# Performance work log

Hardware: AMD Instinct MI355X
Metric: run time of the kernel (lower is better)

Reference implementation:

```python
import jax, jax.numpy as jnp
import numpy as np

EMBED_DIM = 1024
N_HEADS = 16
HEAD_DIM = EMBED_DIM // N_HEADS


def setup_inputs() -> dict:
    key = jax.random.key(0)
    k_x, k_wi, k_bi, k_wo, k_bo = jax.random.split(key, 5)
    B, N, C = 4, 2048, EMBED_DIM
    scale = 1.0 / np.sqrt(C)
    return {
        "x": jax.random.normal(k_x, (B, N, C), dtype=jnp.float32),
        "w_in": jax.random.normal(k_wi, (C, 3 * C), dtype=jnp.float32) * scale,
        "b_in": jax.random.normal(k_bi, (3 * C,), dtype=jnp.float32) * 0.01,
        "w_out": jax.random.normal(k_wo, (C, C), dtype=jnp.float32) * scale,
        "b_out": jax.random.normal(k_bo, (C,), dtype=jnp.float32) * 0.01,
    }


def reference(x, w_in, b_in, w_out, b_out):
    B, N, C = x.shape
    H, D = N_HEADS, HEAD_DIM
    qkv = x @ w_in + b_in  # (B, N, 3C)
    q, k, v = jnp.split(qkv, 3, axis=-1)
    # (B, H, N, D)
    q = q.reshape(B, N, H, D).transpose(0, 2, 1, 3)
    k = k.reshape(B, N, H, D).transpose(0, 2, 1, 3)
    v = v.reshape(B, N, H, D).transpose(0, 2, 1, 3)
    # Naive attention: full (B,H,N,N) scores, NO sqrt(d) scaling (as in source)
    scores = jnp.einsum("bhnd,bhmd->bhnm", q, k)
    attn = jax.nn.softmax(scores, axis=-1)
    out = jnp.einsum("bhnm,bhmd->bhnd", attn, v)
    out = out.transpose(0, 2, 1, 3).reshape(B, N, C)
    return out @ w_out + b_out
```

## Files before the change

### kernel.cpp

```cpp
#include <hip/hip_runtime.h>
#include <hip/hip_bf16.h>
#include <stdint.h>

typedef __attribute__((ext_vector_type(8))) __bf16 bf8v;
typedef __attribute__((ext_vector_type(4))) float f4v;

#define L2E 1.44269504088896f

__device__ __forceinline__ unsigned short f2bf(float f) {
  union { float f; unsigned u; } v; v.f = f;
  unsigned r = v.u + 0x7fffu + ((v.u >> 16) & 1u);
  return (unsigned short)(r >> 16);
}

__device__ __forceinline__ unsigned pk2bf(float f0, float f1) {
  union { __hip_bfloat162 h; unsigned u; } c;
  c.h = __float22bfloat162_rn(make_float2(f0, f1));
  return c.u;
}

__device__ __forceinline__ float exp2_hw(float x) {
  return __builtin_amdgcn_exp2f(x);
}

__device__ __forceinline__ void gl_lds16(const void* g, void* l) {
  __builtin_amdgcn_global_load_lds(
      (__attribute__((address_space(1))) void*)(g),
      (__attribute__((address_space(3))) void*)(l), 16, 0, 0);
}

__global__ void prep_kernel(const float* __restrict__ x,
                            const float* __restrict__ w_in,
                            const float* __restrict__ w_out,
                            unsigned short* __restrict__ xb,
                            unsigned short* __restrict__ wiT,
                            unsigned short* __restrict__ woT) {
  __shared__ float tile[32][33];
  int bx = blockIdx.x;
  if (bx < 8192) {
    int i = bx * 256 + threadIdx.x;
    float4 v = ((const float4*)x)[i];
    ushort4 o;
    o.x = f2bf(v.x); o.y = f2bf(v.y); o.z = f2bf(v.z); o.w = f2bf(v.w);
    ((ushort4*)xb)[i] = o;
    return;
  }
  int idx = bx - 8192;
  int bxx = idx & 127, byy = idx >> 7;
  const float* in; unsigned short* out; int C, c0;
  if (bxx < 96) { in = w_in;  out = wiT; C = 3072; c0 = bxx * 32; }
  else          { in = w_out; out = woT; C = 1024; c0 = (bxx - 96) * 32; }
  int r0 = byy * 32;
  int tx = threadIdx.x & 31, ty = threadIdx.x >> 5;
#pragma unroll
  for (int j = 0; j < 4; ++j)
    tile[ty + 8 * j][tx] = in[(size_t)(r0 + ty + 8 * j) * C + c0 + tx];
  __syncthreads();
#pragma unroll
  for (int j = 0; j < 4; ++j)
    out[(size_t)(c0 + ty + 8 * j) * 1024 + r0 + tx] = f2bf(tile[tx][ty + 8 * j]);
}

__global__ void transpose_v_kernel(const unsigned short* __restrict__ qkv,
                                   unsigned short* __restrict__ vtg) {
  __shared__ unsigned short tile[32][33];
  int bh = blockIdx.z;
  int d0 = blockIdx.y * 32;
  int n0 = blockIdx.x * 32;
  int b = bh >> 4, h = bh & 15;
  int tx = threadIdx.x, ty = threadIdx.y;
  const unsigned short* src = qkv + (size_t)b * 2048 * 3072 + 2048 + h * 64 + d0;
#pragma unroll
  for (int j = 0; j < 4; ++j)
    tile[ty + 8 * j][tx] = src[(size_t)(n0 + ty + 8 * j) * 3072 + tx];
  __syncthreads();
  unsigned short* dst = vtg + ((size_t)bh * 64) * 2048;
#pragma unroll
  for (int j = 0; j < 4; ++j)
    dst[(size_t)(d0 + ty + 8 * j) * 2048 + n0 + tx] = tile[tx][ty + 8 * j];
}

__global__ __launch_bounds__(512, 2) void gemm_bt256(
    const unsigned short* __restrict__ A,
    const unsigned short* __restrict__ BT,
    const float* __restrict__ bias,
    unsigned short* __restrict__ C,
    int N, int K, int nbx, int scale_ncols, float scale) {
  __shared__ __align__(16) unsigned short As[2][256 * 64];
  __shared__ __align__(16) unsigned short Bs[2][256 * 64];
  const int tid = threadIdx.x;
  const int wave = tid >> 6, lane = tid & 63;
  const int lo = lane & 15, hi = lane >> 4;
  const int wm = wave >> 2, wn = wave & 3;

  const int nwg = gridDim.x;
  const int cpx = nwg >> 3;
  const int s = (blockIdx.x & 7) * cpx + (blockIdx.x >> 3);
  const int by = s / nbx, bx = s - by * nbx;
  const int m0 = by * 256, n0 = bx * 256;

  const int srow = lane >> 3;
  const int scol = ((lane & 7) * 8) ^ ((lane >> 1) & 16);
  const unsigned short* gA = A + (size_t)(m0 + wave * 8 + srow) * K + scol;
  const unsigned short* gB = BT + (size_t)(n0 + wave * 8 + srow) * K + scol;

  const int colsw0 = (hi * 8) ^ ((lo & 4) << 2);
  const int colsw1 = (32 + hi * 8) ^ ((lo & 4) << 2);
  const int rA = wm * 128 + lo;
  const int rB = wn * 64 + lo;

  f4v acc[8][4] = {};
  const int nt = K >> 6;

#pragma unroll
  for (int j = 0; j < 4; ++j) {
    gl_lds16(gA + (size_t)(j * 64) * K, &As[0][(j * 64 + wave * 8) * 64]);
    gl_lds16(gB + (size_t)(j * 64) * K, &Bs[0][(j * 64 + wave * 8) * 64]);
  }

  for (int t = 0; t < nt; ++t) {
    const int c = t & 1;
    __builtin_amdgcn_s_barrier();
    __builtin_amdgcn_sched_barrier(0);
    if (t + 1 < nt) {
      const unsigned short* gA1 = gA + (size_t)(t + 1) * 64;
      const unsigned short* gB1 = gB + (size_t)(t + 1) * 64;
#pragma unroll
      for (int j = 0; j < 4; ++j) {
        gl_lds16(gA1 + (size_t)(j * 64) * K, &As[c ^ 1][(j * 64 + wave * 8) * 64]);
        gl_lds16(gB1 + (size_t)(j * 64) * K, &Bs[c ^ 1][(j * 64 + wave * 8) * 64]);
      }
      asm volatile("s_waitcnt vmcnt(8)" ::: "memory");
    } else {
      asm volatile("s_waitcnt vmcnt(0)" ::: "memory");
    }
    __builtin_amdgcn_sched_barrier(0);
    __builtin_amdgcn_s_barrier();
    __builtin_amdgcn_sched_barrier(0);

    bf8v b[4][2];
#pragma unroll
    for (int fn = 0; fn < 4; ++fn) {
      b[fn][0] = *(const bf8v*)&Bs[c][(rB + fn * 16) * 64 + colsw0];
      b[fn][1] = *(const bf8v*)&Bs[c][(rB + fn * 16) * 64 + colsw1];
    }
#pragma unroll
    for (int p = 0; p < 4; ++p) {
      bf8v a[2][2];
#pragma unroll
      for (int i = 0; i < 2; ++i) {
        a[i][0] = *(const bf8v*)&As[c][(rA + (p * 2 + i) * 16) * 64 + colsw0];
        a[i][1] = *(const bf8v*)&As[c][(rA + (p * 2 + i) * 16) * 64 + colsw1];
      }
      __builtin_amdgcn_s_setprio(1);
#pragma unroll
      for (int ks = 0; ks < 2; ++ks)
#pragma unroll
        for (int i = 0; i < 2; ++i)
#pragma unroll
          for (int fn = 0; fn < 4; ++fn)
            acc[p * 2 + i][fn] = __builtin_amdgcn_mfma_f32_16x16x32_bf16(
                a[i][ks], b[fn][ks], acc[p * 2 + i][fn], 0, 0, 0);
      __builtin_amdgcn_s_setprio(0);
    }
  }

#pragma unroll
  for (int i = 0; i < 8; ++i) {
#pragma unroll
    for (int r = 0; r < 4; ++r) {
      int row = m0 + wm * 128 + i * 16 + hi * 4 + r;
#pragma unroll
      for (int j = 0; j < 4; ++j) {
        int col = n0 + wn * 64 + j * 16 + lo;
        float v = acc[i][j][r] + bias[col];
        if (col < scale_ncols) v *= scale;
        C[(size_t)row * N + col] = f2bf(v);
      }
    }
  }
}

__global__ __launch_bounds__(256, 4) void gemm_bt_sm(
    const unsigned short* __restrict__ A,
    const unsigned short* __restrict__ BT,
    const float* __restrict__ bias,
    float* __restrict__ C,
    int M, int N, int K) {
  __shared__ __align__(16) unsigned short As[64 * 32];
  __shared__ __align__(16) unsigned short Bs[128 * 32];
  const int tid = threadIdx.x;
  const int wave = tid >> 6, lane = tid & 63;
  const int lo = lane & 15, hi = lane >> 4;
  const int m0 = blockIdx.y * 64, n0 = blockIdx.x * 128;
  const int wm = (wave >> 1) * 32, wn = (wave & 1) * 64;

  f4v acc[2][4] = {};

  const int srow = lane >> 2;
  const int scol = (lane & 3) * 8;

  for (int k0 = 0; k0 < K; k0 += 32) {
    gl_lds16(A + (size_t)(m0 + wave * 16 + srow) * K + k0 + scol,
             &As[(wave * 16) * 32]);
#pragma unroll
    for (int p = 0; p < 2; ++p) {
      int r = p * 64 + wave * 16 + srow;
      gl_lds16(BT + (size_t)(n0 + r) * K + k0 + scol,
               &Bs[(p * 64 + wave * 16) * 32]);
    }
    __syncthreads();
    bf8v a[2], b[4];
#pragma unroll
    for (int i = 0; i < 2; ++i)
      a[i] = *(const bf8v*)&As[(wm + i * 16 + lo) * 32 + hi * 8];
#pragma unroll
    for (int j = 0; j < 4; ++j)
      b[j] = *(const bf8v*)&Bs[(wn + j * 16 + lo) * 32 + hi * 8];
#pragma unroll
    for (int i = 0; i < 2; ++i)
#pragma unroll
      for (int j = 0; j < 4; ++j)
        acc[i][j] = __builtin_amdgcn_mfma_f32_16x16x32_bf16(a[i], b[j], acc[i][j], 0, 0, 0);
    __syncthreads();
  }

#pragma unroll
  for (int i = 0; i < 2; ++i) {
#pragma unroll
    for (int r = 0; r < 4; ++r) {
      int row = m0 + wm + i * 16 + hi * 4 + r;
#pragma unroll
      for (int j = 0; j < 4; ++j) {
        int col = n0 + wn + j * 16 + lo;
        C[(size_t)row * N + col] = acc[i][j][r] + bias[col];
      }
    }
  }
}

#define FSTR 72

__global__ __launch_bounds__(256, 2) void flash_attn(
    const unsigned short* __restrict__ qkv,
    const unsigned short* __restrict__ vtg,
    unsigned short* __restrict__ y) {
  __shared__ __align__(16) unsigned short Ps[256 * FSTR];
  __shared__ __align__(16) unsigned short Kt[64 * FSTR];
  __shared__ __align__(16) unsigned short Vt[64 * FSTR];
  const int tid = threadIdx.x;
  const int wave = tid >> 6, lane = tid & 63;
  const int lo = lane & 15, hi = lane >> 4;

  const int lin = blockIdx.x;
  const int swz = (lin & 7) * 64 + (lin >> 3);
  const int q0 = (swz & 7) << 8;
  const int h  = (swz >> 3) & 15;
  const int b  = swz >> 7;

  const size_t base = (size_t)b * 2048 * 3072;
  const int qoff = h * 64, koff = 1024 + h * 64;
  const unsigned short* vsrc = vtg + (size_t)(b * 16 + h) * 64 * 2048;

  const int m_st = tid >> 3, c_st = tid & 7;
  const unsigned short* kg = qkv + base + koff;
  float4 rk0, rk1, rv0, rv1;
  auto kv_load = [&](int kt) {
    const int mb = kt * 64;
    rk0 = *(const float4*)(kg + (size_t)(mb + m_st) * 3072 + c_st * 8);
    rk1 = *(const float4*)(kg + (size_t)(mb + m_st + 32) * 3072 + c_st * 8);
    rv0 = *(const float4*)(vsrc + (size_t)m_st * 2048 + mb + c_st * 8);
    rv1 = *(const float4*)(vsrc + (size_t)(m_st + 32) * 2048 + mb + c_st * 8);
  };
  auto kv_write = [&]() {
    *(float4*)&Kt[m_st * FSTR + c_st * 8] = rk0;
    *(float4*)&Kt[(m_st + 32) * FSTR + c_st * 8] = rk1;
    *(float4*)&Vt[m_st * FSTR + c_st * 8] = rv0;
    *(float4*)&Vt[(m_st + 32) * FSTR + c_st * 8] = rv1;
  };

  kv_load(0);

#pragma unroll
  for (int i = 0; i < 8; ++i) {
    int cid = i * 256 + tid;
    int m = cid >> 3, c = cid & 7;
    *(float4*)&Ps[m * FSTR + c * 8] =
        *(const float4*)(qkv + base + (size_t)(q0 + m) * 3072 + qoff + c * 8);
  }
  __syncthreads();
  bf8v bq[4][2];
#pragma unroll
  for (int qt = 0; qt < 4; ++qt)
#pragma unroll
    for (int ks = 0; ks < 2; ++ks)
      bq[qt][ks] = *(const bf8v*)&Ps[(wave * 64 + qt * 16 + lo) * FSTR + ks * 32 + hi * 8];

  f4v O[4][4] = {};
  f4v acc_l[4] = {};
  union { bf8v v; unsigned short u[8]; } onesu;
#pragma unroll
  for (int i = 0; i < 8; ++i) onesu.u[i] = 0x3F80;
  const bf8v ones = onesu.v;

  for (int kt = 0; kt < 32; ++kt) {
    asm volatile("" ::: "memory");
    __builtin_amdgcn_s_barrier();
    asm volatile("" ::: "memory");
    kv_write();
    if (kt < 31) kv_load(kt + 1);
    asm volatile("s_waitcnt lgkmcnt(0)" ::: "memory");
    __builtin_amdgcn_s_barrier();
    asm volatile("" ::: "memory");

#pragma unroll
    for (int ct = 0; ct < 4; ++ct) {
      f4v s[4] = {{}, {}, {}, {}};
      __builtin_amdgcn_s_setprio(1);
#pragma unroll
      for (int ks = 0; ks < 2; ++ks) {
        bf8v ak = *(const bf8v*)&Kt[(ct * 16 + lo) * FSTR + ks * 32 + hi * 8];
#pragma unroll
        for (int qt = 0; qt < 4; ++qt)
          s[qt] = __builtin_amdgcn_mfma_f32_16x16x32_bf16(ak, bq[qt][ks], s[qt], 0, 0, 0);
      }
      __builtin_amdgcn_s_setprio(0);
#pragma unroll
      for (int qt = 0; qt < 4; ++qt) {
        float p0 = exp2_hw(s[qt][0]), p1 = exp2_hw(s[qt][1]);
        float p2 = exp2_hw(s[qt][2]), p3 = exp2_hw(s[qt][3]);
        uint2 w; w.x = pk2bf(p0, p1); w.y = pk2bf(p2, p3);
        *(uint2*)&Ps[(wave * 64 + qt * 16 + lo) * FSTR + ct * 16 + hi * 4] = w;
      }
    }

#pragma unroll
    for (int ks = 0; ks < 2; ++ks) {
      bf8v ap[4];
#pragma unroll
      for (int qt = 0; qt < 4; ++qt)
        ap[qt] = *(const bf8v*)&Ps[(wave * 64 + qt * 16 + lo) * FSTR + ks * 32 + hi * 8];
      __builtin_amdgcn_s_setprio(1);
#pragma unroll
      for (int qt = 0; qt < 4; ++qt)
        acc_l[qt] = __builtin_amdgcn_mfma_f32_16x16x32_bf16(ap[qt], ones, acc_l[qt], 0, 0, 0);
#pragma unroll
      for (int dt = 0; dt < 4; ++dt) {
        bf8v bv = *(const bf8v*)&Vt[(dt * 16 + lo) * FSTR + ks * 32 + hi * 8];
#pragma unroll
        for (int qt = 0; qt < 4; ++qt)
          O[qt][dt] = __builtin_amdgcn_mfma_f32_16x16x32_bf16(ap[qt], bv, O[qt][dt], 0, 0, 0);
      }
      __builtin_amdgcn_s_setprio(0);
    }
  }

#pragma unroll
  for (int qt = 0; qt < 4; ++qt) {
#pragma unroll
    for (int r = 0; r < 4; ++r) {
      float inv = 1.f / acc_l[qt][r];
      int row = q0 + wave * 64 + qt * 16 + hi * 4 + r;
      size_t orow = ((size_t)b * 2048 + row) * 1024 + h * 64;
#pragma unroll
      for (int dt = 0; dt < 4; ++dt)
        y[orow + dt * 16 + lo] = f2bf(O[qt][dt][r] * inv);
    }
  }
}

extern "C" void kernel_launch(void* const* d_in, const int* in_sizes, int n_in,
                              void* d_out, int out_size, void* d_ws, size_t ws_size,
                              hipStream_t stream) {
  (void)in_sizes; (void)n_in; (void)out_size; (void)ws_size;
  const float* x     = (const float*)d_in[0];
  const float* w_in  = (const float*)d_in[1];
  const float* b_in  = (const float*)d_in[2];
  const float* w_out = (const float*)d_in[3];
  const float* b_out = (const float*)d_in[4];

  unsigned short* xb  = (unsigned short*)d_ws;
  unsigned short* wiT = xb  + (size_t)8192 * 1024;
  unsigned short* woT = wiT + (size_t)3072 * 1024;
  unsigned short* qkv = woT + (size_t)1024 * 1024;
  unsigned short* yb  = qkv + (size_t)8192 * 3072;
  unsigned short* vtg = xb;

  prep_kernel<<<12288, 256, 0, stream>>>(x, w_in, w_out, xb, wiT, woT);

  gemm_bt256<<<384, 512, 0, stream>>>(xb, wiT, b_in, qkv, 3072, 1024, 12, 1024, L2E);
  transpose_v_kernel<<<dim3(64, 2, 64), dim3(32, 8), 0, stream>>>(qkv, vtg);
  flash_attn<<<512, 256, 0, stream>>>(qkv, vtg, yb);
  gemm_bt_sm<<<dim3(8, 128), 256, 0, stream>>>(yb, woT, b_out, (float*)d_out,
                                               8192, 1024, 1024);
}
```

Before: 294.4 us.

## Use 256x128 pipelined GEMM for both projections and double-buffer K/V in attention

Turns the big GEMM into a template with a 256x128 tile, a new XOR swizzle and a smaller LDS footprint, and launches it for both the QKV projection (768 blocks) and the output projection in place of the small 64x128 single-buffered kernel. The flash attention kernel now double-buffers the K/V LDS tiles, so each step has one barrier instead of two and the next tile's register-to-LDS write overlaps compute. The aim is better occupancy and load balance for the QKV GEMM, a pipelined output GEMM, and less sync stall in attention. In exchange, the QKV GEMM reuses less data per block and attention uses more LDS.

```diff
diff --git a/kernel.cpp b/kernel.cpp
--- a/kernel.cpp
+++ b/kernel.cpp
@@ -28,6 +28,9 @@
       (__attribute__((address_space(1))) void*)(g),
       (__attribute__((address_space(3))) void*)(l), 16, 0, 0);
 }
+
+__device__ __forceinline__ void store_out(unsigned short* p, float v) { *p = f2bf(v); }
+__device__ __forceinline__ void store_out(float* p, float v) { *p = v; }
 
 __global__ void prep_kernel(const float* __restrict__ x,
                             const float* __restrict__ w_in,
@@ -80,43 +83,44 @@
     dst[(size_t)(d0 + ty + 8 * j) * 2048 + n0 + tx] = tile[tx][ty + 8 * j];
 }
 
-__global__ __launch_bounds__(512, 2) void gemm_bt256(
+template <typename OutT, bool SCALE>
+__global__ __launch_bounds__(512, 2) void gemm256(
     const unsigned short* __restrict__ A,
     const unsigned short* __restrict__ BT,
     const float* __restrict__ bias,
-    unsigned short* __restrict__ C,
+    OutT* __restrict__ C,
     int N, int K, int nbx, int scale_ncols, float scale) {
   __shared__ __align__(16) unsigned short As[2][256 * 64];
-  __shared__ __align__(16) unsigned short Bs[2][256 * 64];
+  __shared__ __align__(16) unsigned short Bs[2][128 * 64];
   const int tid = threadIdx.x;
   const int wave = tid >> 6, lane = tid & 63;
   const int lo = lane & 15, hi = lane >> 4;
-  const int wm = wave >> 2, wn = wave & 3;
-
-  const int nwg = gridDim.x;
-  const int cpx = nwg >> 3;
+  const int wm = wave >> 1, wn = wave & 1;
+
+  const int cpx = gridDim.x >> 3;
   const int s = (blockIdx.x & 7) * cpx + (blockIdx.x >> 3);
   const int by = s / nbx, bx = s - by * nbx;
-  const int m0 = by * 256, n0 = bx * 256;
+  const int m0 = by * 256, n0 = bx * 128;
 
   const int srow = lane >> 3;
-  const int scol = ((lane & 7) * 8) ^ ((lane >> 1) & 16);
+  const int scol = (((lane & 7) ^ (srow & 7)) * 8);
   const unsigned short* gA = A + (size_t)(m0 + wave * 8 + srow) * K + scol;
   const unsigned short* gB = BT + (size_t)(n0 + wave * 8 + srow) * K + scol;
 
-  const int colsw0 = (hi * 8) ^ ((lo & 4) << 2);
-  const int colsw1 = (32 + hi * 8) ^ ((lo & 4) << 2);
-  const int rA = wm * 128 + lo;
-  const int rB = wn * 64 + lo;
-
-  f4v acc[8][4] = {};
+  const int csw0 = ((hi ^ (lo & 7)) * 8);
+  const int csw1 = (((4 + hi) ^ (lo & 7)) * 8);
+  const int rA = wm * 64;
+  const int rB = wn * 64;
+
+  f4v acc[4][4] = {};
   const int nt = K >> 6;
 
 #pragma unroll
-  for (int j = 0; j < 4; ++j) {
+  for (int j = 0; j < 4; ++j)
     gl_lds16(gA + (size_t)(j * 64) * K, &As[0][(j * 64 + wave * 8) * 64]);
+#pragma unroll
+  for (int j = 0; j < 2; ++j)
     gl_lds16(gB + (size_t)(j * 64) * K, &Bs[0][(j * 64 + wave * 8) * 64]);
-  }
 
   for (int t = 0; t < nt; ++t) {
     const int c = t & 1;
@@ -126,11 +130,12 @@
       const unsigned short* gA1 = gA + (size_t)(t + 1) * 64;
       const unsigned short* gB1 = gB + (size_t)(t + 1) * 64;
 #pragma unroll
-      for (int j = 0; j < 4; ++j) {
+      for (int j = 0; j < 4; ++j)
         gl_lds16(gA1 + (size_t)(j * 64) * K, &As[c ^ 1][(j * 64 + wave * 8) * 64]);
+#pragma unroll
+      for (int j = 0; j < 2; ++j)
         gl_lds16(gB1 + (size_t)(j * 64) * K, &Bs[c ^ 1][(j * 64 + wave * 8) * 64]);
-      }
-      asm volatile("s_waitcnt vmcnt(8)" ::: "memory");
+      asm volatile("s_waitcnt vmcnt(6)" ::: "memory");
     } else {
       asm volatile("s_waitcnt vmcnt(0)" ::: "memory");
     }
@@ -141,16 +146,16 @@
     bf8v b[4][2];
 #pragma unroll
     for (int fn = 0; fn < 4; ++fn) {
-      b[fn][0] = *(const bf8v*)&Bs[c][(rB + fn * 16) * 64 + colsw0];
-      b[fn][1] = *(const bf8v*)&Bs[c][(rB + fn * 16) * 64 + colsw1];
-    }
-#pragma unroll
-    for (int p = 0; p < 4; ++p) {
+      b[fn][0] = *(const bf8v*)&Bs[c][(rB + fn * 16 + lo) * 64 + csw0];
+      b[fn][1] = *(const bf8v*)&Bs[c][(rB + fn * 16 + lo) * 64 + csw1];
+    }
+#pragma unroll
+    for (int p = 0; p < 2; ++p) {
       bf8v a[2][2];
 #pragma unroll
       for (int i = 0; i < 2; ++i) {
-        a[i][0] = *(const bf8v*)&As[c][(rA + (p * 2 + i) * 16) * 64 + colsw0];
-        a[i][1] = *(const bf8v*)&As[c][(rA + (p * 2 + i) * 16) * 64 + colsw1];
+        a[i][0] = *(const bf8v*)&As[c][(rA + (p * 2 + i) * 16 + lo) * 64 + csw0];
+        a[i][1] = *(const bf8v*)&As[c][(rA + (p * 2 + i) * 16 + lo) * 64 + csw1];
       }
       __builtin_amdgcn_s_setprio(1);
 #pragma unroll
@@ -166,74 +171,16 @@
   }
 
 #pragma unroll
-  for (int i = 0; i < 8; ++i) {
+  for (int i = 0; i < 4; ++i) {
 #pragma unroll
     for (int r = 0; r < 4; ++r) {
-      int row = m0 + wm * 128 + i * 16 + hi * 4 + r;
+      int row = m0 + wm * 64 + i * 16 + hi * 4 + r;
 #pragma unroll
       for (int j = 0; j < 4; ++j) {
         int col = n0 + wn * 64 + j * 16 + lo;
         float v = acc[i][j][r] + bias[col];
-        if (col < scale_ncols) v *= scale;
-        C[(size_t)row * N + col] = f2bf(v);
-      }
-    }
-  }
-}
-
-__global__ __launch_bounds__(256, 4) void gemm_bt_sm(
-    const unsigned short* __restrict__ A,
-    const unsigned short* __restrict__ BT,
-    const float* __restrict__ bias,
-    float* __restrict__ C,
-    int M, int N, int K) {
-  __shared__ __align__(16) unsigned short As[64 * 32];
-  __shared__ __align__(16) unsigned short Bs[128 * 32];
-  const int tid = threadIdx.x;
-  const int wave = tid >> 6, lane = tid & 63;
-  const int lo = lane & 15, hi = lane >> 4;
-  const int m0 = blockIdx.y * 64, n0 = blockIdx.x * 128;
-  const int wm = (wave >> 1) * 32, wn = (wave & 1) * 64;
-
-  f4v acc[2][4] = {};
-
-  const int srow = lane >> 2;
-  const int scol = (lane & 3) * 8;
-
-  for (int k0 = 0; k0 < K; k0 += 32) {
-    gl_lds16(A + (size_t)(m0 + wave * 16 + srow) * K + k0 + scol,
-             &As[(wave * 16) * 32]);
-#pragma unroll
-    for (int p = 0; p < 2; ++p) {
-      int r = p * 64 + wave * 16 + srow;
-      gl_lds16(BT + (size_t)(n0 + r) * K + k0 + scol,
-               &Bs[(p * 64 + wave * 16) * 32]);
-    }
-    __syncthreads();
-    bf8v a[2], b[4];
-#pragma unroll
-    for (int i = 0; i < 2; ++i)
-      a[i] = *(const bf8v*)&As[(wm + i * 16 + lo) * 32 + hi * 8];
-#pragma unroll
-    for (int j = 0; j < 4; ++j)
-      b[j] = *(const bf8v*)&Bs[(wn + j * 16 + lo) * 32 + hi * 8];
-#pragma unroll
-    for (int i = 0; i < 2; ++i)
-#pragma unroll
-      for (int j = 0; j < 4; ++j)
-        acc[i][j] = __builtin_amdgcn_mfma_f32_16x16x32_bf16(a[i], b[j], acc[i][j], 0, 0, 0);
-    __syncthreads();
-  }
-
-#pragma unroll
-  for (int i = 0; i < 2; ++i) {
-#pragma unroll
-    for (int r = 0; r < 4; ++r) {
-      int row = m0 + wm + i * 16 + hi * 4 + r;
-#pragma unroll
-      for (int j = 0; j < 4; ++j) {
-        int col = n0 + wn + j * 16 + lo;
-        C[(size_t)row * N + col] = acc[i][j][r] + bias[col];
+        if (SCALE && col < scale_ncols) v *= scale;
+        store_out(&C[(size_t)row * N + col], v);
       }
     }
   }
@@ -246,8 +193,8 @@
     const unsigned short* __restrict__ vtg,
     unsigned short* __restrict__ y) {
   __shared__ __align__(16) unsigned short Ps[256 * FSTR];
-  __shared__ __align__(16) unsigned short Kt[64 * FSTR];
-  __shared__ __align__(16) unsigned short Vt[64 * FSTR];
+  __shared__ __align__(16) unsigned short Kt[2][64 * FSTR];
+  __shared__ __align__(16) unsigned short Vt[2][64 * FSTR];
   const int tid = threadIdx.x;
   const int wave = tid >> 6, lane = tid & 63;
   const int lo = lane & 15, hi = lane >> 4;
@@ -272,11 +219,11 @@
     rv0 = *(const float4*)(vsrc + (size_t)m_st * 2048 + mb + c_st * 8);
     rv1 = *(const float4*)(vsrc + (size_t)(m_st + 32) * 2048 + mb + c_st * 8);
   };
-  auto kv_write = [&]() {
-    *(float4*)&Kt[m_st * FSTR + c_st * 8] = rk0;
-    *(float4*)&Kt[(m_st + 32) * FSTR + c_st * 8] = rk1;
-    *(float4*)&Vt[m_st * FSTR + c_st * 8] = rv0;
-    *(float4*)&Vt[(m_st + 32) * FSTR + c_st * 8] = rv1;
+  auto kv_write = [&](int buf) {
+    *(float4*)&Kt[buf][m_st * FSTR + c_st * 8] = rk0;
+    *(float4*)&Kt[buf][(m_st + 32) * FSTR + c_st * 8] = rk1;
+    *(float4*)&Vt[buf][m_st * FSTR + c_st * 8] = rv0;
+    *(float4*)&Vt[buf][(m_st + 32) * FSTR + c_st * 8] = rv1;
   };
 
   kv_load(0);
@@ -303,15 +250,18 @@
   for (int i = 0; i < 8; ++i) onesu.u[i] = 0x3F80;
   const bf8v ones = onesu.v;
 
+  kv_write(0);
+  kv_load(1);
+  asm volatile("s_waitcnt lgkmcnt(0)" ::: "memory");
+  __builtin_amdgcn_s_barrier();
+  asm volatile("" ::: "memory");
+
   for (int kt = 0; kt < 32; ++kt) {
-    asm volatile("" ::: "memory");
-    __builtin_amdgcn_s_barrier();
-    asm volatile("" ::: "memory");
-    kv_write();
-    if (kt < 31) kv_load(kt + 1);
-    asm volatile("s_waitcnt lgkmcnt(0)" ::: "memory");
-    __builtin_amdgcn_s_barrier();
-    asm volatile("" ::: "memory");
+    const int c = kt & 1;
+    if (kt < 31) {
+      kv_write(c ^ 1);
+      if (kt < 30) kv_load(kt + 2);
+    }
 
 #pragma unroll
     for (int ct = 0; ct < 4; ++ct) {
@@ -319,7 +269,7 @@
       __builtin_amdgcn_s_setprio(1);
 #pragma unroll
       for (int ks = 0; ks < 2; ++ks) {
-        bf8v ak = *(const bf8v*)&Kt[(ct * 16 + lo) * FSTR + ks * 32 + hi * 8];
+        bf8v ak = *(const bf8v*)&Kt[c][(ct * 16 + lo) * FSTR + ks * 32 + hi * 8];
 #pragma unroll
         for (int qt = 0; qt < 4; ++qt)
           s[qt] = __builtin_amdgcn_mfma_f32_16x16x32_bf16(ak, bq[qt][ks], s[qt], 0, 0, 0);
@@ -346,13 +296,17 @@
         acc_l[qt] = __builtin_amdgcn_mfma_f32_16x16x32_bf16(ap[qt], ones, acc_l[qt], 0, 0, 0);
 #pragma unroll
       for (int dt = 0; dt < 4; ++dt) {
-        bf8v bv = *(const bf8v*)&Vt[(dt * 16 + lo) * FSTR + ks * 32 + hi * 8];
+        bf8v bv = *(const bf8v*)&Vt[c][(dt * 16 + lo) * FSTR + ks * 32 + hi * 8];
 #pragma unroll
         for (int qt = 0; qt < 4; ++qt)
           O[qt][dt] = __builtin_amdgcn_mfma_f32_16x16x32_bf16(ap[qt], bv, O[qt][dt], 0, 0, 0);
       }
       __builtin_amdgcn_s_setprio(0);
     }
+
+    asm volatile("s_waitcnt lgkmcnt(0)" ::: "memory");
+    __builtin_amdgcn_s_barrier();
+    asm volatile("" ::: "memory");
   }
 
 #pragma unroll
@@ -388,9 +342,10 @@
 
   prep_kernel<<<12288, 256, 0, stream>>>(x, w_in, w_out, xb, wiT, woT);
 
-  gemm_bt256<<<384, 512, 0, stream>>>(xb, wiT, b_in, qkv, 3072, 1024, 12, 1024, L2E);
+  gemm256<unsigned short, true><<<768, 512, 0, stream>>>(
+      xb, wiT, b_in, qkv, 3072, 1024, 24, 1024, L2E);
   transpose_v_kernel<<<dim3(64, 2, 64), dim3(32, 8), 0, stream>>>(qkv, vtg);
   flash_attn<<<512, 256, 0, stream>>>(qkv, vtg, yb);
-  gemm_bt_sm<<<dim3(8, 128), 256, 0, stream>>>(yb, woT, b_out, (float*)d_out,
-                                               8192, 1024, 1024);
-}
+  gemm256<float, false><<<256, 512, 0, stream>>>(
+      yb, woT, b_out, (float*)d_out, 1024, 1024, 8, 0, 1.0f);
+}
```

Measured after the change: 278.6 us. 5.4% less time.
